# Kernel optimization log

Hardware: AMD Instinct MI355X
Metric: run time of the kernel (lower is better)

The kernel has to match this reference:

```python
import jax, jax.numpy as jnp
import numpy as np

OUT_H, OUT_W = 7, 7
SPATIAL_SCALE = 0.0625


def setup_inputs() -> dict:
    key = jax.random.key(0)
    kf, kb, kx, ky, kw, kh = jax.random.split(key, 6)
    B, C, H, W = 2, 256, 38, 38
    n_rois = 64
    features = jax.random.normal(kf, (B, C, H, W), dtype=jnp.float32)
    bidx = jax.random.randint(kb, (n_rois,), 0, B)
    x1 = jax.random.randint(kx, (n_rois,), 0, 300)
    y1 = jax.random.randint(ky, (n_rois,), 0, 300)
    x2 = x1 + jax.random.randint(kw, (n_rois,), 32, 300)  # x2 < 600
    y2 = y1 + jax.random.randint(kh, (n_rois,), 32, 300)
    rois = jnp.stack([bidx, x1, y1, x2, y2], axis=1).astype(jnp.int32)
    return {"features": features, "rois": rois}


def _roi_max_pool(features, rois):
    # features: [B,C,H,W]; rois: [N,5] int (batch_idx,x1,y1,x2,y2) in image coords
    B, C, H, W = features.shape
    ridx = rois[:, 0]
    start_w = rois[:, 1].astype(jnp.float32) * SPATIAL_SCALE
    start_h = rois[:, 2].astype(jnp.float32) * SPATIAL_SCALE
    end_w = rois[:, 3].astype(jnp.float32) * SPATIAL_SCALE
    end_h = rois[:, 4].astype(jnp.float32) * SPATIAL_SCALE
    bin_h = jnp.maximum(end_h - start_h, 1.0) / OUT_H  # [N]
    bin_w = jnp.maximum(end_w - start_w, 1.0) / OUT_W

    oh = jnp.arange(OUT_H, dtype=jnp.float32)
    ow = jnp.arange(OUT_W, dtype=jnp.float32)
    # per-roi per-bin [start,end) extents, clipped to feature map (matches floor/ceil+clamp)
    hs = jnp.clip(jnp.floor(oh[None, :] * bin_h[:, None] + start_h[:, None]).astype(jnp.int32), 0, H)
    he = jnp.clip(jnp.ceil((oh[None, :] + 1.0) * bin_h[:, None] + start_h[:, None]).astype(jnp.int32), 0, H)
    ws = jnp.clip(jnp.floor(ow[None, :] * bin_w[:, None] + start_w[:, None]).astype(jnp.int32), 0, W)
    we = jnp.clip(jnp.ceil((ow[None, :] + 1.0) * bin_w[:, None] + start_w[:, None]).astype(jnp.int32), 0, W)

    hgrid = jnp.arange(H)
    wgrid = jnp.arange(W)
    mask_h = (hgrid[None, None, :] >= hs[:, :, None]) & (hgrid[None, None, :] < he[:, :, None])  # [N,oh,H]
    mask_w = (wgrid[None, None, :] >= ws[:, :, None]) & (wgrid[None, None, :] < we[:, :, None])  # [N,ow,W]

    feat = features[ridx]  # [N,C,H,W] gather per roi
    neg = jnp.float32(-jnp.inf)
    # separable masked max: first over W -> [N,C,H,ow]
    t = jnp.where(mask_w[:, None, None, :, :], feat[:, :, :, None, :], neg).max(axis=-1)
    # then over H -> [N,C,oh,ow]
    out = jnp.where(mask_h[:, None, :, :, None], t[:, :, None, :, :], neg).max(axis=3)
    # empty bins (h_end<=h_start or w_end<=w_start) stay zero in the original
    valid = mask_h.any(-1)[:, None, :, None] & mask_w.any(-1)[:, None, None, :]  # [N,1,oh,ow]
    return jnp.where(valid, out, jnp.float32(0.0))


def reference(features, rois):
    return _roi_max_pool(features, rois)
```

## Files before the change

### kernel.cpp

```cpp
#include <hip/hip_runtime.h>

#define OUT_HW 7
#define NCH    256
#define FH     38
#define FW     38
#define PLANE  (FH * FW)
#define PLANE4 (PLANE / 4)
#define PLANE_PAD4 364


__global__ __launch_bounds__(256) void roi_pool_kernel(
    const float* __restrict__ feat,
    const int*   __restrict__ rois,
    float*       __restrict__ out)
{
    __shared__ float4 lds4[4][PLANE_PAD4];

    int tid  = threadIdx.x;
    int wv   = tid >> 6;
    int lane = tid & 63;
    int p    = blockIdx.x * 4 + wv;
    int c    = p & (NCH - 1);
    int r    = p >> 8;

    const int* roi = rois + r * 5;
    int ridx = roi[0];

    const float4* src4 = (const float4*)(feat + ((size_t)ridx * NCH + c) * PLANE);
    float4* dst4 = &lds4[wv][0];
    #pragma unroll
    for (int i = 0; i < 6; ++i) {
        int j = lane + i * 64;
        if (j < PLANE4) dst4[j] = src4[j];
    }
    __syncthreads();

    if (lane >= OUT_HW * OUT_HW) return;
    int oh = lane / OUT_HW;
    int ow = lane - oh * OUT_HW;

    float sw = (float)roi[1] * 0.0625f;
    float sh = (float)roi[2] * 0.0625f;
    float ew = (float)roi[3] * 0.0625f;
    float eh = (float)roi[4] * 0.0625f;

    const float C7 = __uint_as_float(0x3E124925u);
    float bw = __fmul_rn(fmaxf(ew - sw, 1.0f), C7);
    float bh = __fmul_rn(fmaxf(eh - sh, 1.0f), C7);

    int hs = (int)floorf(fmaf((float)oh,       bh, sh));
    int he = (int)ceilf (fmaf((float)(oh + 1), bh, sh));
    int ws = (int)floorf(fmaf((float)ow,       bw, sw));
    int we = (int)ceilf (fmaf((float)(ow + 1), bw, sw));

    hs = min(max(hs, 0), FH);
    he = min(max(he, 0), FH);
    ws = min(max(ws, 0), FW);
    we = min(max(we, 0), FW);

    float m = 0.0f;
    if (hs < he && ws < we) {
        m = -INFINITY;
        const float* pl = (const float*)&lds4[wv][0];
        for (int h = hs; h < he; ++h) {
            const float* row = pl + h * FW;
            for (int w = ws; w < we; ++w) {
                m = fmaxf(m, row[w]);
            }
        }
    }
    out[(size_t)p * (OUT_HW * OUT_HW) + lane] = m;
}

extern "C" void kernel_launch(void* const* d_in, const int* in_sizes, int n_in,
                              void* d_out, int out_size, void* d_ws, size_t ws_size,
                              hipStream_t stream) {
    const float* feat = (const float*)d_in[0];
    const int*   rois = (const int*)d_in[1];
    float*       out  = (float*)d_out;

    int planes = out_size / (OUT_HW * OUT_HW);
    int blocks = planes / 4;
    roi_pool_kernel<<<blocks, 256, 0, stream>>>(feat, rois, out);
}
```

Measured before the change: 63.11 us.

## Share both batch feature planes per channel across a group of eight ROIs

Each block now loads one channel's planes for both batch images into LDS and computes all bins for eight ROIs, instead of each wavefront loading the plane for a single ROI/channel. This cuts redundant global reads of feature planes, since ROIs that share a batch and channel reuse the same LDS copy. All 256 threads now do bin work (392 outputs per block) rather than only 49 of 64 lanes. The kernel hardcodes a batch size of two and needs the ROI count to divide by eight. Grid size drops by half, which may reduce occupancy.

Measured after the change: 62.00 us. No clear change (-1.8%).

```diff
diff --git a/kernel.cpp b/kernel.cpp
--- a/kernel.cpp
+++ b/kernel.cpp
@@ -1,12 +1,16 @@
 #include <hip/hip_runtime.h>
 
 #define OUT_HW 7
+#define BINS   (OUT_HW * OUT_HW)
 #define NCH    256
+#define NB     2
 #define FH     38
 #define FW     38
 #define PLANE  (FH * FW)
 #define PLANE4 (PLANE / 4)
 #define PLANE_PAD4 364
+#define PLANE_PADF (PLANE_PAD4 * 4)
+#define RPB    8
 
 
 __global__ __launch_bounds__(256) void roi_pool_kernel(
@@ -14,62 +18,71 @@
     const int*   __restrict__ rois,
     float*       __restrict__ out)
 {
-    __shared__ float4 lds4[4][PLANE_PAD4];
+    __shared__ float4 lds4[NB * PLANE_PAD4];
+    __shared__ int    ldsroi[RPB * 5];
 
-    int tid  = threadIdx.x;
-    int wv   = tid >> 6;
-    int lane = tid & 63;
-    int p    = blockIdx.x * 4 + wv;
-    int c    = p & (NCH - 1);
-    int r    = p >> 8;
+    int tid = threadIdx.x;
+    int c   = blockIdx.x & (NCH - 1);
+    int g   = blockIdx.x >> 8;
+    int r0  = g * RPB;
 
-    const int* roi = rois + r * 5;
-    int ridx = roi[0];
+    if (tid < RPB * 5) ldsroi[tid] = rois[r0 * 5 + tid];
 
-    const float4* src4 = (const float4*)(feat + ((size_t)ridx * NCH + c) * PLANE);
-    float4* dst4 = &lds4[wv][0];
+    const float4* src0 = (const float4*)(feat + (size_t)c * PLANE);
+    const float4* src1 = (const float4*)(feat + ((size_t)NCH + c) * PLANE);
     #pragma unroll
-    for (int i = 0; i < 6; ++i) {
-        int j = lane + i * 64;
-        if (j < PLANE4) dst4[j] = src4[j];
+    for (int i = 0; i < 2; ++i) {
+        int j = tid + i * 256;
+        if (j < PLANE4) {
+            lds4[j]              = src0[j];
+            lds4[PLANE_PAD4 + j] = src1[j];
+        }
     }
     __syncthreads();
 
-    if (lane >= OUT_HW * OUT_HW) return;
-    int oh = lane / OUT_HW;
-    int ow = lane - oh * OUT_HW;
+    const float* lf = (const float*)lds4;
 
-    float sw = (float)roi[1] * 0.0625f;
-    float sh = (float)roi[2] * 0.0625f;
-    float ew = (float)roi[3] * 0.0625f;
-    float eh = (float)roi[4] * 0.0625f;
+    #pragma unroll
+    for (int o = tid; o < RPB * BINS; o += 256) {
+        int lr   = o / BINS;
+        int bin  = o - lr * BINS;
+        int oh   = bin / OUT_HW;
+        int ow   = bin - oh * OUT_HW;
+        const int* roi = &ldsroi[lr * 5];
+        int ridx = roi[0];
 
-    const float C7 = __uint_as_float(0x3E124925u);
-    float bw = __fmul_rn(fmaxf(ew - sw, 1.0f), C7);
-    float bh = __fmul_rn(fmaxf(eh - sh, 1.0f), C7);
+        float sw = (float)roi[1] * 0.0625f;
+        float sh = (float)roi[2] * 0.0625f;
+        float ew = (float)roi[3] * 0.0625f;
+        float eh = (float)roi[4] * 0.0625f;
 
-    int hs = (int)floorf(fmaf((float)oh,       bh, sh));
-    int he = (int)ceilf (fmaf((float)(oh + 1), bh, sh));
-    int ws = (int)floorf(fmaf((float)ow,       bw, sw));
-    int we = (int)ceilf (fmaf((float)(ow + 1), bw, sw));
+        const float C7 = __uint_as_float(0x3E124925u);
+        float bw = __fmul_rn(fmaxf(ew - sw, 1.0f), C7);
+        float bh = __fmul_rn(fmaxf(eh - sh, 1.0f), C7);
 
-    hs = min(max(hs, 0), FH);
-    he = min(max(he, 0), FH);
-    ws = min(max(ws, 0), FW);
-    we = min(max(we, 0), FW);
+        int hs = (int)floorf(fmaf((float)oh,       bh, sh));
+        int he = (int)ceilf (fmaf((float)(oh + 1), bh, sh));
+        int ws = (int)floorf(fmaf((float)ow,       bw, sw));
+        int we = (int)ceilf (fmaf((float)(ow + 1), bw, sw));
 
-    float m = 0.0f;
-    if (hs < he && ws < we) {
-        m = -INFINITY;
-        const float* pl = (const float*)&lds4[wv][0];
-        for (int h = hs; h < he; ++h) {
-            const float* row = pl + h * FW;
-            for (int w = ws; w < we; ++w) {
-                m = fmaxf(m, row[w]);
+        hs = min(max(hs, 0), FH);
+        he = min(max(he, 0), FH);
+        ws = min(max(ws, 0), FW);
+        we = min(max(we, 0), FW);
+
+        float m = 0.0f;
+        if (hs < he && ws < we) {
+            m = -INFINITY;
+            const float* pl = lf + ridx * PLANE_PADF;
+            for (int h = hs; h < he; ++h) {
+                const float* row = pl + h * FW;
+                for (int w = ws; w < we; ++w) {
+                    m = fmaxf(m, row[w]);
+                }
             }
         }
+        out[((size_t)((r0 + lr) * NCH + c)) * BINS + bin] = m;
     }
-    out[(size_t)p * (OUT_HW * OUT_HW) + lane] = m;
 }
 
 extern "C" void kernel_launch(void* const* d_in, const int* in_sizes, int n_in,
@@ -79,7 +92,7 @@
     const int*   rois = (const int*)d_in[1];
     float*       out  = (float*)d_out;
 
-    int planes = out_size / (OUT_HW * OUT_HW);
-    int blocks = planes / 4;
-    roi_pool_kernel<<<blocks, 256, 0, stream>>>(feat, rois, out);
+    int n_rois = out_size / (BINS * NCH);
+    int groups = n_rois / RPB;
+    roi_pool_kernel<<<dim3(NCH * groups), 256, 0, stream>>>(feat, rois, out);
 }
```

## Drop LDS plane staging and read bins directly from global memory

Applied to the files above, without the earlier changes.

Removes the per-wave copy of the full feature plane into shared memory and the barrier. Each thread now computes one output bin and reads only its window from global memory, with one thread per output element and no idle lanes. This avoids loading plane regions outside the ROI, which matters since many ROIs are clipped or small. In exchange, reads become scattered and uncoalesced, and overlapping bins re-read data through the cache.

After: 64.03 us. About the same (+1.5%).

```diff
diff --git a/kernel.cpp b/kernel.cpp
--- a/kernel.cpp
+++ b/kernel.cpp
@@ -1,43 +1,31 @@
 #include <hip/hip_runtime.h>
 
 #define OUT_HW 7
+#define BINS   (OUT_HW * OUT_HW)
 #define NCH    256
 #define FH     38
 #define FW     38
 #define PLANE  (FH * FW)
-#define PLANE4 (PLANE / 4)
-#define PLANE_PAD4 364
 
 
 __global__ __launch_bounds__(256) void roi_pool_kernel(
     const float* __restrict__ feat,
     const int*   __restrict__ rois,
-    float*       __restrict__ out)
+    float*       __restrict__ out,
+    int total)
 {
-    __shared__ float4 lds4[4][PLANE_PAD4];
+    int o = blockIdx.x * 256 + threadIdx.x;
+    if (o >= total) return;
 
-    int tid  = threadIdx.x;
-    int wv   = tid >> 6;
-    int lane = tid & 63;
-    int p    = blockIdx.x * 4 + wv;
-    int c    = p & (NCH - 1);
-    int r    = p >> 8;
+    int p   = o / BINS;
+    int bin = o - p * BINS;
+    int r   = p >> 8;
+    int c   = p & (NCH - 1);
+    int oh  = bin / OUT_HW;
+    int ow  = bin - oh * OUT_HW;
 
     const int* roi = rois + r * 5;
     int ridx = roi[0];
-
-    const float4* src4 = (const float4*)(feat + ((size_t)ridx * NCH + c) * PLANE);
-    float4* dst4 = &lds4[wv][0];
-    #pragma unroll
-    for (int i = 0; i < 6; ++i) {
-        int j = lane + i * 64;
-        if (j < PLANE4) dst4[j] = src4[j];
-    }
-    __syncthreads();
-
-    if (lane >= OUT_HW * OUT_HW) return;
-    int oh = lane / OUT_HW;
-    int ow = lane - oh * OUT_HW;
 
     float sw = (float)roi[1] * 0.0625f;
     float sh = (float)roi[2] * 0.0625f;
@@ -61,7 +49,7 @@
     float m = 0.0f;
     if (hs < he && ws < we) {
         m = -INFINITY;
-        const float* pl = (const float*)&lds4[wv][0];
+        const float* pl = feat + ((size_t)ridx * NCH + c) * PLANE;
         for (int h = hs; h < he; ++h) {
             const float* row = pl + h * FW;
             for (int w = ws; w < we; ++w) {
@@ -69,7 +57,7 @@
             }
         }
     }
-    out[(size_t)p * (OUT_HW * OUT_HW) + lane] = m;
+    out[o] = m;
 }
 
 extern "C" void kernel_launch(void* const* d_in, const int* in_sizes, int n_in,
@@ -79,7 +67,6 @@
     const int*   rois = (const int*)d_in[1];
     float*       out  = (float*)d_out;
 
-    int planes = out_size / (OUT_HW * OUT_HW);
-    int blocks = planes / 4;
-    roi_pool_kernel<<<blocks, 256, 0, stream>>>(feat, rois, out);
+    int blocks = (out_size + 255) / 256;
+    roi_pool_kernel<<<blocks, 256, 0, stream>>>(feat, rois, out, out_size);
 }
```
